# Kernel tuning notes

Hardware: AMD Instinct MI355X
Metric: run time of the kernel (lower is better)

Reference implementation:

```python
import jax, jax.numpy as jnp
import numpy as np

# Pauli-Z expectation table: sign of bit w in 4-bit index (wire 0 = MSB, axis order q0..q3)
_idx = np.arange(16)
_bits = (_idx[None, :] >> (3 - np.arange(4))[:, None]) & 1
_Z_TABLE = (1.0 - 2.0 * _bits).astype(np.float32)  # (4, 16)


def _apply_ry(state, theta, wire):
    # state: (N, 2,2,2,2) real amplitudes; RY = [[c,-s],[s,c]], c=cos(t/2), s=sin(t/2)
    ax = 1 + wire
    c = jnp.cos(theta / 2)
    s = jnp.sin(theta / 2)
    st = jnp.moveaxis(state, ax, 1)
    s0, s1 = st[:, 0], st[:, 1]
    st = jnp.stack([c * s0 - s * s1, s * s0 + c * s1], axis=1)
    return jnp.moveaxis(st, 1, ax)


def _apply_cnot(state, control, target):
    # flips the target axis on the control==1 slice (assumes target > control)
    ac, at = 1 + control, 1 + target
    s0 = jnp.take(state, 0, axis=ac)
    s1 = jnp.flip(jnp.take(state, 1, axis=ac), axis=at - 1)
    return jnp.stack([s0, s1], axis=ac)


def setup_inputs() -> dict:
    key = jax.random.key(0)
    ks = jax.random.split(key, 8)
    B = 8192
    x = jax.random.uniform(ks[0], (B, 1, 28, 28), dtype=jnp.float32)
    conv_w = jax.random.normal(ks[1], (4, 1, 2, 2), dtype=jnp.float32) * 0.5
    conv_b = jax.random.normal(ks[2], (4,), dtype=jnp.float32) * 0.1
    bn_gamma = jnp.ones((4,), jnp.float32)
    bn_beta = jnp.zeros((4,), jnp.float32)
    bn_mean = jnp.zeros((4,), jnp.float32)
    bn_var = jnp.ones((4,), jnp.float32)
    shortcut_weight = jnp.float32(1.0)
    theta = jax.random.normal(ks[3], (8,), dtype=jnp.float32)  # 8 trainable RY angles
    lin_w = jax.random.normal(ks[4], (10, 784), dtype=jnp.float32) * 0.03
    lin_b = jnp.zeros((10,), jnp.float32)
    log_scale = jnp.float32(1.0)
    return {"x": x, "conv_w": conv_w, "conv_b": conv_b, "bn_gamma": bn_gamma,
            "bn_beta": bn_beta, "bn_mean": bn_mean, "bn_var": bn_var,
            "shortcut_weight": shortcut_weight, "theta": theta,
            "lin_w": lin_w, "lin_b": lin_b, "log_scale": log_scale}


def reference(x, conv_w, conv_b, bn_gamma, bn_beta, bn_mean, bn_var,
              shortcut_weight, theta, lin_w, lin_b, log_scale):
    B = x.shape[0]
    # classical shortcut: conv(1->4, k2, s2) + BN (eval mode, running stats)
    sc = jax.lax.conv_general_dilated(
        x, conv_w, window_strides=(2, 2), padding='VALID',
        dimension_numbers=('NCHW', 'OIHW', 'NCHW')) + conv_b[None, :, None, None]
    sc = (sc - bn_mean[None, :, None, None]) * jax.lax.rsqrt(bn_var[None, :, None, None] + 1e-5)
    sc = sc * bn_gamma[None, :, None, None] + bn_beta[None, :, None, None]
    sc = sc.reshape(B, -1)  # (B, 784) channel-major, matches torch .view

    # extract 2x2 patches in (r, c) scan order -> (B*196, 4) with order [tl, tr, bl, br]
    img = x.reshape(B, 28, 28)
    patches = img.reshape(B, 14, 2, 14, 2).transpose(0, 1, 3, 2, 4).reshape(B * 196, 4)

    # RY encoding of |0000>: product state, amplitudes [cos(v/2), sin(v/2)] per wire
    half = patches * 0.5
    e = jnp.stack([jnp.cos(half), jnp.sin(half)], axis=-1)  # (N, 4, 2)
    state = jnp.einsum('na,nb,nc,nd->nabcd', e[:, 0], e[:, 1], e[:, 2], e[:, 3])

    # parameterized circuit: RY layer, CNOT(0,1), CNOT(2,3), RY layer
    for w in range(4):
        state = _apply_ry(state, theta[w], w)
    state = _apply_cnot(state, 0, 1)
    state = _apply_cnot(state, 2, 3)
    for w in range(4):
        state = _apply_ry(state, theta[4 + w], w)

    # <Z_w> expectations (real amplitudes -> probs = state**2)
    probs = (state ** 2).reshape(-1, 16)        # (B*196, 16)
    meas = probs @ jnp.asarray(_Z_TABLE).T      # (B*196, 4)
    qfeat = meas.reshape(B, 196 * 4)            # cat order: patch-major, wires inner

    feat = shortcut_weight * sc + qfeat
    logits = (feat @ lin_w.T + lin_b) * log_scale  # dropout is identity in eval
    return jax.nn.log_softmax(logits, axis=-1)
```

## Files before the change

### kernel.cpp

```cpp
#include <hip/hip_runtime.h>
#include <hip/hip_fp16.h>
#include <math.h>

#define BLOCK 512
#define WVS   8

typedef _Float16 h2v __attribute__((ext_vector_type(2)));

__device__ __forceinline__ float dot2h(unsigned a, unsigned b, float c) {
#if __has_builtin(__builtin_amdgcn_fdot2)
    return __builtin_amdgcn_fdot2(__builtin_bit_cast(h2v, a),
                                  __builtin_bit_cast(h2v, b), c, false);
#else
    h2v xa = __builtin_bit_cast(h2v, a), yb = __builtin_bit_cast(h2v, b);
    return c + (float)xa[0] * (float)yb[0] + (float)xa[1] * (float)yb[1];
#endif
}

__device__ __forceinline__ unsigned packh(float a, float b) {
    __half2 h = __float22half2_rn(make_float2(a, b));
    return __builtin_bit_cast(unsigned, h);
}

__device__ __forceinline__ unsigned pkadd(unsigned a, unsigned b) {
    __half2 r = __hadd2(__builtin_bit_cast(__half2, a), __builtin_bit_cast(__half2, b));
    return __builtin_bit_cast(unsigned, r);
}

__device__ __forceinline__ float rfl(float v) {
    return __builtin_bit_cast(float,
        __builtin_amdgcn_readfirstlane(__builtin_bit_cast(int, v)));
}

__device__ __forceinline__ void nsincos(float r, float& s, float& c) {
#if __has_builtin(__builtin_amdgcn_sinf) && __has_builtin(__builtin_amdgcn_cosf) && __has_builtin(__builtin_amdgcn_fractf)
    float rf = __builtin_amdgcn_fractf(r);
    s = __builtin_amdgcn_sinf(rf);
    c = __builtin_amdgcn_cosf(rf);
#else
    float rf = r - floorf(r);
    __sincosf(rf * 6.2831853071795864f, &s, &c);
#endif
}

template <int CTRL, int RMASK>
__device__ __forceinline__ float dppadd(float x) {
    int t = __builtin_amdgcn_update_dpp(0, __builtin_bit_cast(int, x),
                                        CTRL, RMASK, 0xf, false);
    return x + __builtin_bit_cast(float, t);
}
__device__ __forceinline__ float wave_sum64(float x) {
    x = dppadd<0x111, 0xf>(x);
    x = dppadd<0x112, 0xf>(x);
    x = dppadd<0x114, 0xf>(x);
    x = dppadd<0x118, 0xf>(x);
    x = dppadd<0x142, 0xa>(x);
    x = dppadd<0x143, 0xc>(x);
    return __builtin_bit_cast(float,
        __builtin_amdgcn_readlane(__builtin_bit_cast(int, x), 63));
}

__device__ __forceinline__ float sel10(const float L[10], int j) {
    float a0 = (j & 1) ? L[1] : L[0];
    float a2 = (j & 1) ? L[3] : L[2];
    float a4 = (j & 1) ? L[5] : L[4];
    float a6 = (j & 1) ? L[7] : L[6];
    float a8 = (j & 1) ? L[9] : L[8];
    float b0 = (j & 2) ? a2 : a0;
    float b4 = (j & 2) ? a6 : a4;
    float c0 = (j & 4) ? b4 : b0;
    return (j & 8) ? a8 : c0;
}

__global__ __launch_bounds__(BLOCK, 8) void quanv_fused6(
    const float* __restrict__ x,
    const float* __restrict__ conv_w,
    const float* __restrict__ conv_b,
    const float* __restrict__ bn_gamma,
    const float* __restrict__ bn_beta,
    const float* __restrict__ bn_mean,
    const float* __restrict__ bn_var,
    const float* __restrict__ sw_p,
    const float* __restrict__ theta,
    const float* __restrict__ lin_w,
    const float* __restrict__ lin_b,
    const float* __restrict__ log_scale_p,
    float* __restrict__ out)
{
    __shared__ __half lw2[5 * 196 * 8];
    __shared__ __half fsc[WVS][784];

    const int t = threadIdx.x;
    const int lane = t & 63, wv = t >> 6;
    const int img = blockIdx.x * WVS + wv;
    const float INV2PI = 0.15915494309189535f;

    const float* xb = x + (size_t)img * 784;
    float2 px[4][2];
#pragma unroll
    for (int j = 0; j < 4; ++j) {
        int p = (j < 3) ? (lane + 64 * j) : (192 + (lane & 3));
        int i = p / 14, jj = p - i * 14;
        const int off = i * 56 + jj * 2;
        px[j][0] = *(const float2*)(xb + off);
        px[j][1] = *(const float2*)(xb + off + 28);
    }

    for (int q = t; q < 1960; q += BLOCK) {
        float4 v = *(const float4*)(lin_w + q * 4);
        int k = q / 196;
        int p = q - k * 196;
        uint2 pk;
        pk.x = packh(v.x, v.y);
        pk.y = packh(v.z, v.w);
        *(uint2*)&lw2[(k >> 1) * 1568 + p * 8 + (k & 1) * 4] = pk;
    }

    const float sw = sw_p[0];
    const float ls = rfl(log_scale_p[0]);
    float wfS[16], bfS[4];
#pragma unroll
    for (int c = 0; c < 4; ++c) {
        float scale = bn_gamma[c] * rsqrtf(bn_var[c] + 1e-5f);
        float sws = sw * scale;
#pragma unroll
        for (int k = 0; k < 4; ++k) wfS[c * 4 + k] = rfl(sws * conv_w[c * 4 + k]);
        bfS[c] = rfl(sw * (scale * (conv_b[c] - bn_mean[c]) + bn_beta[c]));
    }
    float thc[4];
#pragma unroll
    for (int w = 0; w < 4; ++w) thc[w] = rfl(theta[w] * INV2PI);
    float sE0, cE0, sF0, cF0, sE1, cE1, sF1, cF1;
    {
        float s, c;
        nsincos(theta[4] * INV2PI, s, c); sE0 = rfl(s); cE0 = rfl(c);
        nsincos(theta[5] * INV2PI, s, c); sF0 = rfl(s); cF0 = rfl(c);
        nsincos(theta[6] * INV2PI, s, c); sE1 = rfl(s); cE1 = rfl(c);
        nsincos(theta[7] * INV2PI, s, c); sF1 = rfl(s); cF1 = rfl(c);
    }

    unsigned qr[4][2];
#pragma unroll
    for (int j = 0; j < 4; ++j) {
        if (j == 3 && lane >= 4) break;
        const int p = (j < 3) ? (lane + 64 * j) : (192 + lane);
        const float x00 = px[j][0].x, x01 = px[j][0].y;
        const float x10 = px[j][1].x, x11 = px[j][1].y;
        float sa, ca, sb, cb;
        nsincos(fmaf(x00, INV2PI, thc[0]), sa, ca);
        nsincos(fmaf(x01, INV2PI, thc[1]), sb, cb);
        const float m0 = cE0 * ca - sE0 * (sa * sb);
        const float m1 = cF0 * (ca * cb) - sF0 * sb;
        nsincos(fmaf(x10, INV2PI, thc[2]), sa, ca);
        nsincos(fmaf(x11, INV2PI, thc[3]), sb, cb);
        const float m2 = cE1 * ca - sE1 * (sa * sb);
        const float m3 = cF1 * (ca * cb) - sF1 * sb;
        qr[j][0] = packh(m0, m1);
        qr[j][1] = packh(m2, m3);
#pragma unroll
        for (int c = 0; c < 4; ++c) {
            float v = fmaf(wfS[c * 4 + 0], x00,
                      fmaf(wfS[c * 4 + 1], x01,
                      fmaf(wfS[c * 4 + 2], x10,
                      fmaf(wfS[c * 4 + 3], x11, bfS[c]))));
            fsc[wv][c * 196 + p] = __float2half(v);
        }
    }

    __syncthreads();

    float acc[10];
#pragma unroll
    for (int k = 0; k < 10; ++k) acc[k] = 0.f;

#pragma unroll
    for (int j = 0; j < 4; ++j) {
        if (j == 3 && lane >= 4) break;
        const int p = (j < 3) ? (lane + 64 * j) : (192 + lane);
        uint2 f = *(const uint2*)&fsc[wv][4 * p];
        const unsigned fa0 = pkadd(f.x, qr[j][0]);
        const unsigned fa1 = pkadd(f.y, qr[j][1]);
        const __half* wbase = &lw2[p * 8];
#pragma unroll
        for (int kk = 0; kk < 5; ++kk) {
            uint4 w = *(const uint4*)&wbase[kk * 1568];
            acc[2 * kk]     = dot2h(fa0, w.x, acc[2 * kk]);
            acc[2 * kk]     = dot2h(fa1, w.y, acc[2 * kk]);
            acc[2 * kk + 1] = dot2h(fa0, w.z, acc[2 * kk + 1]);
            acc[2 * kk + 1] = dot2h(fa1, w.w, acc[2 * kk + 1]);
        }
    }

    float L[10];
#pragma unroll
    for (int k = 0; k < 10; ++k)
        L[k] = (wave_sum64(acc[k]) + lin_b[k]) * ls;

    float m = L[0];
#pragma unroll
    for (int k = 1; k < 10; ++k) m = fmaxf(m, L[k]);
    float e = 0.f;
#pragma unroll
    for (int k = 0; k < 10; ++k) e += __expf(L[k] - m);
    const float lse = m + __logf(e);

    if (lane < 10)
        out[(size_t)img * 10 + lane] = sel10(L, lane) - lse;
}

extern "C" void kernel_launch(void* const* d_in, const int* in_sizes, int n_in,
                              void* d_out, int out_size, void* d_ws, size_t ws_size,
                              hipStream_t stream) {
    const float* x         = (const float*)d_in[0];
    const float* conv_w    = (const float*)d_in[1];
    const float* conv_b    = (const float*)d_in[2];
    const float* bn_gamma  = (const float*)d_in[3];
    const float* bn_beta   = (const float*)d_in[4];
    const float* bn_mean   = (const float*)d_in[5];
    const float* bn_var    = (const float*)d_in[6];
    const float* sw        = (const float*)d_in[7];
    const float* theta     = (const float*)d_in[8];
    const float* lin_w     = (const float*)d_in[9];
    const float* lin_b     = (const float*)d_in[10];
    const float* log_scale = (const float*)d_in[11];
    float* out = (float*)d_out;

    const int B = in_sizes[0] / 784;
    dim3 grid(B / WVS), block(BLOCK);
    hipLaunchKernelGGL(quanv_fused6, grid, block, 0, stream,
                       x, conv_w, conv_b, bn_gamma, bn_beta, bn_mean, bn_var,
                       sw, theta, lin_w, lin_b, log_scale, out);
}
```

Before: 21.18 us.

## Process two images per wavefront to amortize LDS weight staging

Each wavefront now handles two images instead of one, which halves the grid. Each block therefore stages the fp16 linear weights into LDS once for 16 images rather than 8. Every weight vector read from LDS is reused for two dot-product accumulations. The costs are higher register pressure, since the min-blocks launch bound was dropped and the accumulators doubled, and half as many blocks for latency hiding.

```diff
diff --git a/kernel.cpp b/kernel.cpp
--- a/kernel.cpp
+++ b/kernel.cpp
@@ -72,7 +72,7 @@
     return (j & 8) ? a8 : c0;
 }
 
-__global__ __launch_bounds__(BLOCK, 8) void quanv_fused6(
+__global__ __launch_bounds__(BLOCK) void quanv_fused8(
     const float* __restrict__ x,
     const float* __restrict__ conv_w,
     const float* __restrict__ conv_b,
@@ -88,22 +88,25 @@
     float* __restrict__ out)
 {
     __shared__ __half lw2[5 * 196 * 8];
-    __shared__ __half fsc[WVS][784];
+    __shared__ __half fsc[WVS][2][784];
 
     const int t = threadIdx.x;
     const int lane = t & 63, wv = t >> 6;
-    const int img = blockIdx.x * WVS + wv;
+    const int img0 = (blockIdx.x * WVS + wv) * 2;
     const float INV2PI = 0.15915494309189535f;
 
-    const float* xb = x + (size_t)img * 784;
-    float2 px[4][2];
+    const float* xb0 = x + (size_t)img0 * 784;
+    const float* xb1 = xb0 + 784;
+    float2 pxa[4][2], pxb[4][2];
 #pragma unroll
     for (int j = 0; j < 4; ++j) {
         int p = (j < 3) ? (lane + 64 * j) : (192 + (lane & 3));
         int i = p / 14, jj = p - i * 14;
         const int off = i * 56 + jj * 2;
-        px[j][0] = *(const float2*)(xb + off);
-        px[j][1] = *(const float2*)(xb + off + 28);
+        pxa[j][0] = *(const float2*)(xb0 + off);
+        pxa[j][1] = *(const float2*)(xb0 + off + 28);
+        pxb[j][0] = *(const float2*)(xb1 + off);
+        pxb[j][1] = *(const float2*)(xb1 + off + 28);
     }
 
     for (int q = t; q < 1960; q += BLOCK) {
@@ -139,73 +142,114 @@
         nsincos(theta[7] * INV2PI, s, c); sF1 = rfl(s); cF1 = rfl(c);
     }
 
-    unsigned qr[4][2];
+    unsigned qra[4][2], qrb[4][2];
 #pragma unroll
     for (int j = 0; j < 4; ++j) {
         if (j == 3 && lane >= 4) break;
         const int p = (j < 3) ? (lane + 64 * j) : (192 + lane);
-        const float x00 = px[j][0].x, x01 = px[j][0].y;
-        const float x10 = px[j][1].x, x11 = px[j][1].y;
-        float sa, ca, sb, cb;
-        nsincos(fmaf(x00, INV2PI, thc[0]), sa, ca);
-        nsincos(fmaf(x01, INV2PI, thc[1]), sb, cb);
-        const float m0 = cE0 * ca - sE0 * (sa * sb);
-        const float m1 = cF0 * (ca * cb) - sF0 * sb;
-        nsincos(fmaf(x10, INV2PI, thc[2]), sa, ca);
-        nsincos(fmaf(x11, INV2PI, thc[3]), sb, cb);
-        const float m2 = cE1 * ca - sE1 * (sa * sb);
-        const float m3 = cF1 * (ca * cb) - sF1 * sb;
-        qr[j][0] = packh(m0, m1);
-        qr[j][1] = packh(m2, m3);
-#pragma unroll
-        for (int c = 0; c < 4; ++c) {
-            float v = fmaf(wfS[c * 4 + 0], x00,
-                      fmaf(wfS[c * 4 + 1], x01,
-                      fmaf(wfS[c * 4 + 2], x10,
-                      fmaf(wfS[c * 4 + 3], x11, bfS[c]))));
-            fsc[wv][c * 196 + p] = __float2half(v);
+        {
+            const float x00 = pxa[j][0].x, x01 = pxa[j][0].y;
+            const float x10 = pxa[j][1].x, x11 = pxa[j][1].y;
+            float sa, ca, sb, cb;
+            nsincos(fmaf(x00, INV2PI, thc[0]), sa, ca);
+            nsincos(fmaf(x01, INV2PI, thc[1]), sb, cb);
+            const float m0 = cE0 * ca - sE0 * (sa * sb);
+            const float m1 = cF0 * (ca * cb) - sF0 * sb;
+            nsincos(fmaf(x10, INV2PI, thc[2]), sa, ca);
+            nsincos(fmaf(x11, INV2PI, thc[3]), sb, cb);
+            const float m2 = cE1 * ca - sE1 * (sa * sb);
+            const float m3 = cF1 * (ca * cb) - sF1 * sb;
+            qra[j][0] = packh(m0, m1);
+            qra[j][1] = packh(m2, m3);
+#pragma unroll
+            for (int c = 0; c < 4; ++c) {
+                float v = fmaf(wfS[c * 4 + 0], x00,
+                          fmaf(wfS[c * 4 + 1], x01,
+                          fmaf(wfS[c * 4 + 2], x10,
+                          fmaf(wfS[c * 4 + 3], x11, bfS[c]))));
+                fsc[wv][0][c * 196 + p] = __float2half(v);
+            }
         }
+        {
+            const float x00 = pxb[j][0].x, x01 = pxb[j][0].y;
+            const float x10 = pxb[j][1].x, x11 = pxb[j][1].y;
+            float sa, ca, sb, cb;
+            nsincos(fmaf(x00, INV2PI, thc[0]), sa, ca);
+            nsincos(fmaf(x01, INV2PI, thc[1]), sb, cb);
+            const float m0 = cE0 * ca - sE0 * (sa * sb);
+            const float m1 = cF0 * (ca * cb) - sF0 * sb;
+            nsincos(fmaf(x10, INV2PI, thc[2]), sa, ca);
+            nsincos(fmaf(x11, INV2PI, thc[3]), sb, cb);
+            const float m2 = cE1 * ca - sE1 * (sa * sb);
+            const float m3 = cF1 * (ca * cb) - sF1 * sb;
+            qrb[j][0] = packh(m0, m1);
+            qrb[j][1] = packh(m2, m3);
+#pragma unroll
+            for (int c = 0; c < 4; ++c) {
+                float v = fmaf(wfS[c * 4 + 0], x00,
+                          fmaf(wfS[c * 4 + 1], x01,
+                          fmaf(wfS[c * 4 + 2], x10,
+                          fmaf(wfS[c * 4 + 3], x11, bfS[c]))));
+                fsc[wv][1][c * 196 + p] = __float2half(v);
+            }
+        }
     }
 
     __syncthreads();
 
-    float acc[10];
-#pragma unroll
-    for (int k = 0; k < 10; ++k) acc[k] = 0.f;
+    float acc0[10], acc1[10];
+#pragma unroll
+    for (int k = 0; k < 10; ++k) { acc0[k] = 0.f; acc1[k] = 0.f; }
 
 #pragma unroll
     for (int j = 0; j < 4; ++j) {
         if (j == 3 && lane >= 4) break;
         const int p = (j < 3) ? (lane + 64 * j) : (192 + lane);
-        uint2 f = *(const uint2*)&fsc[wv][4 * p];
-        const unsigned fa0 = pkadd(f.x, qr[j][0]);
-        const unsigned fa1 = pkadd(f.y, qr[j][1]);
+        uint2 f0 = *(const uint2*)&fsc[wv][0][4 * p];
+        uint2 f1 = *(const uint2*)&fsc[wv][1][4 * p];
+        const unsigned fa0 = pkadd(f0.x, qra[j][0]);
+        const unsigned fa1 = pkadd(f0.y, qra[j][1]);
+        const unsigned fb0 = pkadd(f1.x, qrb[j][0]);
+        const unsigned fb1 = pkadd(f1.y, qrb[j][1]);
         const __half* wbase = &lw2[p * 8];
 #pragma unroll
         for (int kk = 0; kk < 5; ++kk) {
             uint4 w = *(const uint4*)&wbase[kk * 1568];
-            acc[2 * kk]     = dot2h(fa0, w.x, acc[2 * kk]);
-            acc[2 * kk]     = dot2h(fa1, w.y, acc[2 * kk]);
-            acc[2 * kk + 1] = dot2h(fa0, w.z, acc[2 * kk + 1]);
-            acc[2 * kk + 1] = dot2h(fa1, w.w, acc[2 * kk + 1]);
+            acc0[2 * kk]     = dot2h(fa0, w.x, acc0[2 * kk]);
+            acc0[2 * kk]     = dot2h(fa1, w.y, acc0[2 * kk]);
+            acc0[2 * kk + 1] = dot2h(fa0, w.z, acc0[2 * kk + 1]);
+            acc0[2 * kk + 1] = dot2h(fa1, w.w, acc0[2 * kk + 1]);
+            acc1[2 * kk]     = dot2h(fb0, w.x, acc1[2 * kk]);
+            acc1[2 * kk]     = dot2h(fb1, w.y, acc1[2 * kk]);
+            acc1[2 * kk + 1] = dot2h(fb0, w.z, acc1[2 * kk + 1]);
+            acc1[2 * kk + 1] = dot2h(fb1, w.w, acc1[2 * kk + 1]);
         }
     }
 
-    float L[10];
-#pragma unroll
-    for (int k = 0; k < 10; ++k)
-        L[k] = (wave_sum64(acc[k]) + lin_b[k]) * ls;
-
-    float m = L[0];
-#pragma unroll
-    for (int k = 1; k < 10; ++k) m = fmaxf(m, L[k]);
-    float e = 0.f;
-#pragma unroll
-    for (int k = 0; k < 10; ++k) e += __expf(L[k] - m);
-    const float lse = m + __logf(e);
-
+    float L0[10], L1[10];
+#pragma unroll
+    for (int k = 0; k < 10; ++k) {
+        L0[k] = (wave_sum64(acc0[k]) + lin_b[k]) * ls;
+        L1[k] = (wave_sum64(acc1[k]) + lin_b[k]) * ls;
+    }
+
+    float mA = L0[0], mB = L1[0];
+#pragma unroll
+    for (int k = 1; k < 10; ++k) { mA = fmaxf(mA, L0[k]); mB = fmaxf(mB, L1[k]); }
+    float eA = 0.f, eB = 0.f;
+#pragma unroll
+    for (int k = 0; k < 10; ++k) {
+        eA += __expf(L0[k] - mA);
+        eB += __expf(L1[k] - mB);
+    }
+    const float lseA = mA + __logf(eA);
+    const float lseB = mB + __logf(eB);
+
+    const int j = lane & 15;
     if (lane < 10)
-        out[(size_t)img * 10 + lane] = sel10(L, lane) - lse;
+        out[(size_t)img0 * 10 + j] = sel10(L0, j) - lseA;
+    else if (lane >= 16 && lane < 26)
+        out[(size_t)(img0 + 1) * 10 + j] = sel10(L1, j) - lseB;
 }
 
 extern "C" void kernel_launch(void* const* d_in, const int* in_sizes, int n_in,
@@ -226,8 +270,8 @@
     float* out = (float*)d_out;
 
     const int B = in_sizes[0] / 784;
-    dim3 grid(B / WVS), block(BLOCK);
-    hipLaunchKernelGGL(quanv_fused6, grid, block, 0, stream,
+    dim3 grid(B / (WVS * 2)), block(BLOCK);
+    hipLaunchKernelGGL(quanv_fused8, grid, block, 0, stream,
                        x, conv_w, conv_b, bn_gamma, bn_beta, bn_mean, bn_var,
                        sw, theta, lin_w, lin_b, log_scale, out);
 }
```

Result: no change. 21.17 us (-0.0%).
